# Performance work log

Hardware: AMD Instinct MI355X
Metric: run time of the kernel (lower is better)

The kernel has to match this reference:

```python
import jax, jax.numpy as jnp
import numpy as np

N = 10000        # total_node
IN_SIZE = 128
OUT_SIZE = 128


def setup_inputs() -> dict:
    key = jax.random.key(0)
    k_adj, k_x, k_wn, k_ws = jax.random.split(key, 4)
    adj = jax.random.uniform(k_adj, (N, N), dtype=jnp.float32)           # package[1]
    old_node_embedding = jax.random.normal(k_x, (N, IN_SIZE), dtype=jnp.float32)
    # nn.Linear weights are stored [out, in]
    W_nei = jax.random.normal(k_wn, (OUT_SIZE, IN_SIZE), dtype=jnp.float32) * (1.0 / np.sqrt(IN_SIZE))
    W_self = jax.random.normal(k_ws, (OUT_SIZE, IN_SIZE), dtype=jnp.float32) * (1.0 / np.sqrt(IN_SIZE))
    return {
        "adj": adj,
        "old_node_embedding": old_node_embedding,
        "W_nei": W_nei,
        "W_self": W_self,
        "out_size": OUT_SIZE,
        "use_divce": 0,
    }


def reference(adj, old_node_embedding, W_nei, W_self, out_size, use_divce):
    # Vectorized form of the per-node torch loop:
    #   nei_gather[n]   = adj[n, :] @ X                (torch.mm per node)
    #   nei_info[n]     = nei_gather[n] @ W_nei^T      (nei_update1)
    #   self_info[n]    = X[n] @ W_self^T              (self_node_update1)
    #   new_emb[n]      = act(nei_info[n] + self_info[n])
    # active_method fixed to tanh.
    nei_gather = adj @ old_node_embedding                         # [N, in]
    nei_info = nei_gather @ W_nei.T                               # [N, out]
    self_info = old_node_embedding @ W_self.T                     # [N, out]
    return jnp.tanh(nei_info + self_info)
```

## Files before the change

kernel.cpp:

```cpp
#include <hip/hip_runtime.h>
#include <cmath>


#define N_NODES 10000
#define EMB 128
#define XNT_STRIDE 10240
#define KC 800
#define NKCH 13
#define LDSW 40

typedef __bf16 bf16x8 __attribute__((ext_vector_type(8)));
typedef float  f32x4  __attribute__((ext_vector_type(4)));

__device__ __forceinline__ bf16x8 bzero8() {
    bf16x8 v;
#pragma unroll
    for (int i = 0; i < 8; ++i) v[i] = (__bf16)0.0f;
    return v;
}

__global__ __launch_bounds__(256) void prep_kernel(
    const float* __restrict__ X, const float* __restrict__ Wn,
    __bf16* __restrict__ xnt_hi, __bf16* __restrict__ xnt_lo)
{
    __shared__ float Xl[32 * EMB];
    const int tid = threadIdx.x;
    const int n0 = blockIdx.x * 32;

#pragma unroll
    for (int i = 0; i < 4; ++i) {
        int idx = tid + i * 256;
        int r = idx >> 5;
        int c4 = (idx & 31) << 2;
        int row = n0 + r;
        float4 v = make_float4(0.f, 0.f, 0.f, 0.f);
        if (row < N_NODES) v = *(const float4*)(X + (size_t)row * EMB + c4);
        *(float4*)(Xl + r * EMB + c4) = v;
    }
    __syncthreads();

    const int c = tid & 127;
    const int half = tid >> 7;
    const float* wrow = Wn + c * EMB;

    float acc[16];
#pragma unroll
    for (int r = 0; r < 16; ++r) acc[r] = 0.f;

    for (int k4 = 0; k4 < 32; ++k4) {
        float4 w = *(const float4*)(wrow + k4 * 4);
#pragma unroll
        for (int r = 0; r < 16; ++r) {
            float4 x = *(const float4*)(Xl + (half * 16 + r) * EMB + k4 * 4);
            acc[r] += x.x * w.x + x.y * w.y + x.z * w.z + x.w * w.w;
        }
    }

    if (n0 + half * 16 < N_NODES) {
        bf16x8 h0, h1, l0, l1;
#pragma unroll
        for (int r = 0; r < 16; ++r) {
            float f = acc[r];
            __bf16 h = (__bf16)f;
            __bf16 l = (__bf16)(f - (float)h);
            if (r < 8) { h0[r] = h; l0[r] = l; }
            else       { h1[r - 8] = h; l1[r - 8] = l; }
        }
        size_t base = (size_t)c * XNT_STRIDE + n0 + half * 16;
        *(bf16x8*)(xnt_hi + base)     = h0;
        *(bf16x8*)(xnt_hi + base + 8) = h1;
        *(bf16x8*)(xnt_lo + base)     = l0;
        *(bf16x8*)(xnt_lo + base + 8) = l1;
    }
}

__device__ __forceinline__ void g_load(
    const float* __restrict__ arow_p, bool arv,
    const __bf16* __restrict__ bh_p, const __bf16* __restrict__ bl_p,
    int k0, int kc_end, int akq, int bkq, float4 av[4], bf16x8 bv[4])
{
    int ak = k0 + akq * 16;
#pragma unroll
    for (int i = 0; i < 4; ++i) {
        float4 v = make_float4(0.f, 0.f, 0.f, 0.f);
        int k = ak + i * 4;
        if (arv && k < kc_end) v = *(const float4*)(arow_p + k);
        av[i] = v;
    }
    int bk = k0 + bkq * 16;
    if (bk < kc_end) {
        bv[0] = *(const bf16x8*)(bh_p + bk);
        bv[1] = *(const bf16x8*)(bh_p + bk + 8);
        bv[2] = *(const bf16x8*)(bl_p + bk);
        bv[3] = *(const bf16x8*)(bl_p + bk + 8);
    } else {
        bv[0] = bv[1] = bv[2] = bv[3] = bzero8();
    }
}

__global__ __launch_bounds__(256, 2) void gemm_kernel(
    const float* __restrict__ adj, const __bf16* __restrict__ xnt_hi,
    const __bf16* __restrict__ xnt_lo, float* __restrict__ Ppart)
{
    __shared__ __bf16 Ah[128 * LDSW];
    __shared__ __bf16 Al[128 * LDSW];
    __shared__ __bf16 Bh[128 * LDSW];
    __shared__ __bf16 Bl[128 * LDSW];

    const int tid = threadIdx.x;
    const int m0 = blockIdx.x * 128;
    const int kc0 = blockIdx.y * KC;
    const int kc_end = min(kc0 + KC, N_NODES);
    const int nsub = (kc_end - kc0 + 31) >> 5;

    const int lane = tid & 63;
    const int wave = tid >> 6;
    const int wm = (wave & 1) * 64;
    const int wn = (wave >> 1) * 64;
    const int fr = lane & 15;
    const int q = lane >> 4;

    const int am = tid >> 1, akq = tid & 1;
    const bool arv = (m0 + am) < N_NODES;
    const float* arow_p = adj + (size_t)(m0 + am) * N_NODES;
    const int bc = tid >> 1, bkq = tid & 1;
    const __bf16* bh_p = xnt_hi + (size_t)bc * XNT_STRIDE;
    const __bf16* bl_p = xnt_lo + (size_t)bc * XNT_STRIDE;

    f32x4 acc[4][4];
#pragma unroll
    for (int mt = 0; mt < 4; ++mt)
#pragma unroll
        for (int nt = 0; nt < 4; ++nt)
#pragma unroll
            for (int e = 0; e < 4; ++e) acc[mt][nt][e] = 0.f;

    float4 av[4];
    bf16x8 bv[4];
    g_load(arow_p, arv, bh_p, bl_p, kc0, kc_end, akq, bkq, av, bv);

    for (int ks = 0; ks < nsub; ++ks) {
        bf16x8 ahv[2], alv[2];
#pragma unroll
        for (int i = 0; i < 16; ++i) {
            float f = ((const float*)av)[i];
            __bf16 h = (__bf16)f;
            __bf16 l = (__bf16)(f - (float)h);
            ahv[i >> 3][i & 7] = h;
            alv[i >> 3][i & 7] = l;
        }
        *(bf16x8*)&Ah[am * LDSW + akq * 16]     = ahv[0];
        *(bf16x8*)&Ah[am * LDSW + akq * 16 + 8] = ahv[1];
        *(bf16x8*)&Al[am * LDSW + akq * 16]     = alv[0];
        *(bf16x8*)&Al[am * LDSW + akq * 16 + 8] = alv[1];
        *(bf16x8*)&Bh[bc * LDSW + bkq * 16]     = bv[0];
        *(bf16x8*)&Bh[bc * LDSW + bkq * 16 + 8] = bv[1];
        *(bf16x8*)&Bl[bc * LDSW + bkq * 16]     = bv[2];
        *(bf16x8*)&Bl[bc * LDSW + bkq * 16 + 8] = bv[3];
        __syncthreads();

        float4 av2[4];
        bf16x8 bv2[4];
        g_load(arow_p, arv, bh_p, bl_p, kc0 + (ks + 1) * 32, kc_end, akq, bkq, av2, bv2);

        bf16x8 a_h[4], a_l[4], b_h[4], b_l[4];
#pragma unroll
        for (int t = 0; t < 4; ++t) {
            a_h[t] = *(const bf16x8*)&Ah[(wm + t * 16 + fr) * LDSW + q * 8];
            a_l[t] = *(const bf16x8*)&Al[(wm + t * 16 + fr) * LDSW + q * 8];
            b_h[t] = *(const bf16x8*)&Bh[(wn + t * 16 + fr) * LDSW + q * 8];
            b_l[t] = *(const bf16x8*)&Bl[(wn + t * 16 + fr) * LDSW + q * 8];
        }
#pragma unroll
        for (int mt = 0; mt < 4; ++mt)
#pragma unroll
            for (int nt = 0; nt < 4; ++nt) {
                acc[mt][nt] = __builtin_amdgcn_mfma_f32_16x16x32_bf16(a_h[mt], b_h[nt], acc[mt][nt], 0, 0, 0);
                acc[mt][nt] = __builtin_amdgcn_mfma_f32_16x16x32_bf16(a_h[mt], b_l[nt], acc[mt][nt], 0, 0, 0);
                acc[mt][nt] = __builtin_amdgcn_mfma_f32_16x16x32_bf16(a_l[mt], b_h[nt], acc[mt][nt], 0, 0, 0);
            }
        __syncthreads();
#pragma unroll
        for (int i = 0; i < 4; ++i) { av[i] = av2[i]; bv[i] = bv2[i]; }
    }

    float* P = Ppart + (size_t)blockIdx.y * ((size_t)N_NODES * EMB);
#pragma unroll
    for (int mt = 0; mt < 4; ++mt) {
        int rbase = m0 + wm + mt * 16 + q * 4;
#pragma unroll
        for (int nt = 0; nt < 4; ++nt) {
            int col = wn + nt * 16 + fr;
#pragma unroll
            for (int r = 0; r < 4; ++r) {
                int row = rbase + r;
                if (row < N_NODES)
                    P[(size_t)row * EMB + col] = acc[mt][nt][r];
            }
        }
    }
}

__global__ __launch_bounds__(256) void epi_kernel(
    const float* __restrict__ X, const float* __restrict__ Wself,
    const float* __restrict__ Ppart, float* __restrict__ out)
{
    __shared__ float Xl[32 * EMB];
    const int tid = threadIdx.x;
    const int n0 = blockIdx.x * 32;

#pragma unroll
    for (int i = 0; i < 4; ++i) {
        int idx = tid + i * 256;
        int r = idx >> 5;
        int c4 = (idx & 31) << 2;
        int row = n0 + r;
        float4 v = make_float4(0.f, 0.f, 0.f, 0.f);
        if (row < N_NODES) v = *(const float4*)(X + (size_t)row * EMB + c4);
        *(float4*)(Xl + r * EMB + c4) = v;
    }
    __syncthreads();

    const int c = tid & 127;
    const int half = tid >> 7;
    const float* wrow = Wself + c * EMB;

    float acc[16];
#pragma unroll
    for (int r = 0; r < 16; ++r) acc[r] = 0.f;

    for (int k4 = 0; k4 < 32; ++k4) {
        float4 w = *(const float4*)(wrow + k4 * 4);
#pragma unroll
        for (int r = 0; r < 16; ++r) {
            float4 x = *(const float4*)(Xl + (half * 16 + r) * EMB + k4 * 4);
            acc[r] += x.x * w.x + x.y * w.y + x.z * w.z + x.w * w.w;
        }
    }

    if (n0 + half * 16 < N_NODES) {
        const size_t rb = (size_t)(n0 + half * 16) * EMB + c;
#pragma unroll
        for (int p = 0; p < NKCH; ++p) {
            const float* Pp = Ppart + (size_t)p * ((size_t)N_NODES * EMB) + rb;
#pragma unroll
            for (int r = 0; r < 16; ++r)
                acc[r] += Pp[(size_t)r * EMB];
        }
#pragma unroll
        for (int r = 0; r < 16; ++r)
            out[rb + (size_t)r * EMB] = tanhf(acc[r]);
    }
}

__global__ __launch_bounds__(256) void gemm0_kernel(
    const float* __restrict__ adj, const float* __restrict__ X,
    float* __restrict__ Y)
{
    __shared__ float As[128 * 33];
    __shared__ float Xs[32 * 132];
    const int tid = threadIdx.x;
    const int m0 = blockIdx.x * 128;
    const int kc0 = blockIdx.y * KC;
    const int kc_end = min(kc0 + KC, N_NODES);
    const int nsub = (kc_end - kc0 + 31) >> 5;

    const int am = tid >> 1, akq = tid & 1;
    const bool arv = (m0 + am) < N_NODES;
    const float* arow_p = adj + (size_t)(m0 + am) * N_NODES;
    const int xr = tid >> 3, xq = tid & 7;
    const int mq = tid >> 4, nq = tid & 15;

    float acc[8][8];
#pragma unroll
    for (int i = 0; i < 8; ++i)
#pragma unroll
        for (int j = 0; j < 8; ++j) acc[i][j] = 0.f;

    for (int ks = 0; ks < nsub; ++ks) {
        int k0 = kc0 + ks * 32;
#pragma unroll
        for (int i = 0; i < 4; ++i) {
            int k = k0 + akq * 16 + i * 4;
            float4 v = make_float4(0.f, 0.f, 0.f, 0.f);
            if (arv && k < kc_end) v = *(const float4*)(arow_p + k);
            float* d = As + am * 33 + akq * 16 + i * 4;
            d[0] = v.x; d[1] = v.y; d[2] = v.z; d[3] = v.w;
        }
#pragma unroll
        for (int i = 0; i < 4; ++i) {
            int c0 = xq * 16 + i * 4;
            int krow = k0 + xr;
            float4 v = make_float4(0.f, 0.f, 0.f, 0.f);
            if (krow < kc_end) v = *(const float4*)(X + (size_t)krow * EMB + c0);
            *(float4*)(Xs + xr * 132 + c0) = v;
        }
        __syncthreads();
        for (int k = 0; k < 32; ++k) {
            float a8[8];
#pragma unroll
            for (int i = 0; i < 8; ++i) a8[i] = As[(mq * 8 + i) * 33 + k];
            float4 x0 = *(const float4*)(Xs + k * 132 + nq * 8);
            float4 x1 = *(const float4*)(Xs + k * 132 + nq * 8 + 4);
            float x8[8] = { x0.x, x0.y, x0.z, x0.w, x1.x, x1.y, x1.z, x1.w };
#pragma unroll
            for (int i = 0; i < 8; ++i)
#pragma unroll
                for (int j = 0; j < 8; ++j) acc[i][j] += a8[i] * x8[j];
        }
        __syncthreads();
    }
#pragma unroll
    for (int i = 0; i < 8; ++i) {
        int row = m0 + mq * 8 + i;
        if (row < N_NODES) {
#pragma unroll
            for (int j = 0; j < 8; ++j)
                atomicAdd(Y + (size_t)row * EMB + nq * 8 + j, acc[i][j]);
        }
    }
}

__global__ __launch_bounds__(256) void epi0_kernel(
    const float* __restrict__ X, const float* __restrict__ Wn,
    const float* __restrict__ Ws, float* __restrict__ out)
{
    __shared__ float Xl[32 * EMB];
    __shared__ float Yl[32 * EMB];
    const int tid = threadIdx.x;
    const int n0 = blockIdx.x * 32;

#pragma unroll
    for (int i = 0; i < 4; ++i) {
        int idx = tid + i * 256;
        int r = idx >> 5;
        int c4 = (idx & 31) << 2;
        int row = n0 + r;
        float4 vx = make_float4(0.f, 0.f, 0.f, 0.f);
        float4 vy = vx;
        if (row < N_NODES) {
            vx = *(const float4*)(X + (size_t)row * EMB + c4);
            vy = *(const float4*)(out + (size_t)row * EMB + c4);
        }
        *(float4*)(Xl + r * EMB + c4) = vx;
        *(float4*)(Yl + r * EMB + c4) = vy;
    }
    __syncthreads();

    const int c = tid & 127;
    const int half = tid >> 7;
    const float* wn = Wn + c * EMB;
    const float* ws = Ws + c * EMB;

    float accn[16], accs[16];
#pragma unroll
    for (int r = 0; r < 16; ++r) { accn[r] = 0.f; accs[r] = 0.f; }

    for (int k4 = 0; k4 < 32; ++k4) {
        float4 a = *(const float4*)(wn + k4 * 4);
        float4 b = *(const float4*)(ws + k4 * 4);
#pragma unroll
        for (int r = 0; r < 16; ++r) {
            float4 y = *(const float4*)(Yl + (half * 16 + r) * EMB + k4 * 4);
            float4 x = *(const float4*)(Xl + (half * 16 + r) * EMB + k4 * 4);
            accn[r] += y.x * a.x + y.y * a.y + y.z * a.z + y.w * a.w;
            accs[r] += x.x * b.x + x.y * b.y + x.z * b.z + x.w * b.w;
        }
    }
#pragma unroll
    for (int r = 0; r < 16; ++r) {
        int row = n0 + half * 16 + r;
        if (row < N_NODES)
            out[(size_t)row * EMB + c] = tanhf(accn[r] + accs[r]);
    }
}

extern "C" void kernel_launch(void* const* d_in, const int* in_sizes, int n_in,
                              void* d_out, int out_size, void* d_ws, size_t ws_size,
                              hipStream_t stream) {
    const float* adj = (const float*)d_in[0];
    const float* X   = (const float*)d_in[1];
    const float* Wn  = (const float*)d_in[2];
    const float* Ws  = (const float*)d_in[3];
    float* out = (float*)d_out;

    const size_t xnt_elems = (size_t)EMB * XNT_STRIDE;
    const size_t xnt_bytes = xnt_elems * 2 * sizeof(unsigned short);
    const size_t part_bytes = (size_t)NKCH * N_NODES * EMB * sizeof(float);

    if (ws_size >= xnt_bytes + part_bytes) {
        __bf16* xh = (__bf16*)d_ws;
        __bf16* xl = xh + xnt_elems;
        float* Ppart = (float*)((char*)d_ws + xnt_bytes);
        prep_kernel<<<(N_NODES + 31) / 32, 256, 0, stream>>>(X, Wn, xh, xl);
        gemm_kernel<<<dim3((N_NODES + 127) / 128, NKCH), 256, 0, stream>>>(adj, xh, xl, Ppart);
        epi_kernel<<<(N_NODES + 31) / 32, 256, 0, stream>>>(X, Ws, Ppart, out);
    } else {
        hipMemsetAsync(d_out, 0, (size_t)N_NODES * EMB * sizeof(float), stream);
        gemm0_kernel<<<dim3((N_NODES + 127) / 128, NKCH), 256, 0, stream>>>(adj, X, out);
        epi0_kernel<<<(N_NODES + 31) / 32, 256, 0, stream>>>(X, Wn, Ws, out);
    }
}
```

Baseline: 636.5 us.

## Load MFMA fragments directly from global memory, dropping LDS staging and barriers

The GEMM kernel no longer stages adj and X tiles through shared memory. Each lane now loads its own MFMA fragment rows straight from global memory into registers, splits them into bf16 hi/lo in place, and double-buffers in registers, which removes both __syncthreads per k-step. The split-K chunk grows (fewer partial chunks), which shrinks the partial-sum traffic and the reduction. In exchange, adj data is loaded redundantly by the two waves that share the same rows (and B by the two waves sharing columns), and the accesses are less coalesced, so more global or L2 traffic is expected.

```diff
diff --git a/kernel.cpp b/kernel.cpp
--- a/kernel.cpp
+++ b/kernel.cpp
@@ -5,9 +5,8 @@
 #define N_NODES 10000
 #define EMB 128
 #define XNT_STRIDE 10240
-#define KC 800
-#define NKCH 13
-#define LDSW 40
+#define KC 1440
+#define NKCH 7
 
 typedef __bf16 bf16x8 __attribute__((ext_vector_type(8)));
 typedef float  f32x4  __attribute__((ext_vector_type(4)));
@@ -17,6 +16,17 @@
 #pragma unroll
     for (int i = 0; i < 8; ++i) v[i] = (__bf16)0.0f;
     return v;
+}
+
+__device__ __forceinline__ void split8(const float4& x0, const float4& x1,
+                                       bf16x8& h, bf16x8& l) {
+    float f[8] = {x0.x, x0.y, x0.z, x0.w, x1.x, x1.y, x1.z, x1.w};
+#pragma unroll
+    for (int i = 0; i < 8; ++i) {
+        __bf16 hh = (__bf16)f[i];
+        h[i] = hh;
+        l[i] = (__bf16)(f[i] - (float)hh);
+    }
 }
 
 __global__ __launch_bounds__(256) void prep_kernel(
@@ -74,27 +84,34 @@
     }
 }
 
-__device__ __forceinline__ void g_load(
-    const float* __restrict__ arow_p, bool arv,
-    const __bf16* __restrict__ bh_p, const __bf16* __restrict__ bl_p,
-    int k0, int kc_end, int akq, int bkq, float4 av[4], bf16x8 bv[4])
-{
-    int ak = k0 + akq * 16;
-#pragma unroll
-    for (int i = 0; i < 4; ++i) {
-        float4 v = make_float4(0.f, 0.f, 0.f, 0.f);
-        int k = ak + i * 4;
-        if (arv && k < kc_end) v = *(const float4*)(arow_p + k);
-        av[i] = v;
-    }
-    int bk = k0 + bkq * 16;
-    if (bk < kc_end) {
-        bv[0] = *(const bf16x8*)(bh_p + bk);
-        bv[1] = *(const bf16x8*)(bh_p + bk + 8);
-        bv[2] = *(const bf16x8*)(bl_p + bk);
-        bv[3] = *(const bf16x8*)(bl_p + bk + 8);
-    } else {
-        bv[0] = bv[1] = bv[2] = bv[3] = bzero8();
+struct SubTile {
+    float4 a0[4], a1[4];
+    bf16x8 bh[4], bl[4];
+};
+
+__device__ __forceinline__ void load_sub(
+    const float* const (&arow)[4], const bool (&arv)[4],
+    const __bf16* const (&bhp)[4], const __bf16* const (&blp)[4],
+    int k, int kc_end, SubTile& s)
+{
+    const bool kv = k < kc_end;
+#pragma unroll
+    for (int t = 0; t < 4; ++t) {
+        float4 v0 = make_float4(0.f, 0.f, 0.f, 0.f);
+        float4 v1 = v0;
+        if (kv && arv[t]) {
+            v0 = *(const float4*)(arow[t] + k);
+            v1 = *(const float4*)(arow[t] + k + 4);
+        }
+        s.a0[t] = v0;
+        s.a1[t] = v1;
+        bf16x8 h = bzero8(), l = bzero8();
+        if (kv) {
+            h = *(const bf16x8*)(bhp[t] + k);
+            l = *(const bf16x8*)(blp[t] + k);
+        }
+        s.bh[t] = h;
+        s.bl[t] = l;
     }
 }
 
@@ -102,11 +119,6 @@
     const float* __restrict__ adj, const __bf16* __restrict__ xnt_hi,
     const __bf16* __restrict__ xnt_lo, float* __restrict__ Ppart)
 {
-    __shared__ __bf16 Ah[128 * LDSW];
-    __shared__ __bf16 Al[128 * LDSW];
-    __shared__ __bf16 Bh[128 * LDSW];
-    __shared__ __bf16 Bl[128 * LDSW];
-
     const int tid = threadIdx.x;
     const int m0 = blockIdx.x * 128;
     const int kc0 = blockIdx.y * KC;
@@ -118,14 +130,22 @@
     const int wm = (wave & 1) * 64;
     const int wn = (wave >> 1) * 64;
     const int fr = lane & 15;
-    const int q = lane >> 4;
-
-    const int am = tid >> 1, akq = tid & 1;
-    const bool arv = (m0 + am) < N_NODES;
-    const float* arow_p = adj + (size_t)(m0 + am) * N_NODES;
-    const int bc = tid >> 1, bkq = tid & 1;
-    const __bf16* bh_p = xnt_hi + (size_t)bc * XNT_STRIDE;
-    const __bf16* bl_p = xnt_lo + (size_t)bc * XNT_STRIDE;
+    const int q  = lane >> 4;
+    const int q8 = q * 8;
+
+    const float* arow[4];
+    bool arv[4];
+    const __bf16* bhp[4];
+    const __bf16* blp[4];
+#pragma unroll
+    for (int t = 0; t < 4; ++t) {
+        int row = m0 + wm + t * 16 + fr;
+        arv[t] = row < N_NODES;
+        arow[t] = adj + (size_t)(arv[t] ? row : 0) * N_NODES;
+        int col = wn + t * 16 + fr;
+        bhp[t] = xnt_hi + (size_t)col * XNT_STRIDE;
+        blp[t] = xnt_lo + (size_t)col * XNT_STRIDE;
+    }
 
     f32x4 acc[4][4];
 #pragma unroll
@@ -135,53 +155,25 @@
 #pragma unroll
             for (int e = 0; e < 4; ++e) acc[mt][nt][e] = 0.f;
 
-    float4 av[4];
-    bf16x8 bv[4];
-    g_load(arow_p, arv, bh_p, bl_p, kc0, kc_end, akq, bkq, av, bv);
+    SubTile cur, nxt;
+    load_sub(arow, arv, bhp, blp, kc0 + q8, kc_end, cur);
 
     for (int ks = 0; ks < nsub; ++ks) {
-        bf16x8 ahv[2], alv[2];
-#pragma unroll
-        for (int i = 0; i < 16; ++i) {
-            float f = ((const float*)av)[i];
-            __bf16 h = (__bf16)f;
-            __bf16 l = (__bf16)(f - (float)h);
-            ahv[i >> 3][i & 7] = h;
-            alv[i >> 3][i & 7] = l;
-        }
-        *(bf16x8*)&Ah[am * LDSW + akq * 16]     = ahv[0];
-        *(bf16x8*)&Ah[am * LDSW + akq * 16 + 8] = ahv[1];
-        *(bf16x8*)&Al[am * LDSW + akq * 16]     = alv[0];
-        *(bf16x8*)&Al[am * LDSW + akq * 16 + 8] = alv[1];
-        *(bf16x8*)&Bh[bc * LDSW + bkq * 16]     = bv[0];
-        *(bf16x8*)&Bh[bc * LDSW + bkq * 16 + 8] = bv[1];
-        *(bf16x8*)&Bl[bc * LDSW + bkq * 16]     = bv[2];
-        *(bf16x8*)&Bl[bc * LDSW + bkq * 16 + 8] = bv[3];
-        __syncthreads();
-
-        float4 av2[4];
-        bf16x8 bv2[4];
-        g_load(arow_p, arv, bh_p, bl_p, kc0 + (ks + 1) * 32, kc_end, akq, bkq, av2, bv2);
-
-        bf16x8 a_h[4], a_l[4], b_h[4], b_l[4];
-#pragma unroll
-        for (int t = 0; t < 4; ++t) {
-            a_h[t] = *(const bf16x8*)&Ah[(wm + t * 16 + fr) * LDSW + q * 8];
-            a_l[t] = *(const bf16x8*)&Al[(wm + t * 16 + fr) * LDSW + q * 8];
-            b_h[t] = *(const bf16x8*)&Bh[(wn + t * 16 + fr) * LDSW + q * 8];
-            b_l[t] = *(const bf16x8*)&Bl[(wn + t * 16 + fr) * LDSW + q * 8];
-        }
+        load_sub(arow, arv, bhp, blp, kc0 + (ks + 1) * 32 + q8, kc_end, nxt);
+
+        bf16x8 ah[4], al[4];
+#pragma unroll
+        for (int t = 0; t < 4; ++t) split8(cur.a0[t], cur.a1[t], ah[t], al[t]);
+
 #pragma unroll
         for (int mt = 0; mt < 4; ++mt)
 #pragma unroll
             for (int nt = 0; nt < 4; ++nt) {
-                acc[mt][nt] = __builtin_amdgcn_mfma_f32_16x16x32_bf16(a_h[mt], b_h[nt], acc[mt][nt], 0, 0, 0);
-                acc[mt][nt] = __builtin_amdgcn_mfma_f32_16x16x32_bf16(a_h[mt], b_l[nt], acc[mt][nt], 0, 0, 0);
-                acc[mt][nt] = __builtin_amdgcn_mfma_f32_16x16x32_bf16(a_l[mt], b_h[nt], acc[mt][nt], 0, 0, 0);
+                acc[mt][nt] = __builtin_amdgcn_mfma_f32_16x16x32_bf16(ah[mt], cur.bh[nt], acc[mt][nt], 0, 0, 0);
+                acc[mt][nt] = __builtin_amdgcn_mfma_f32_16x16x32_bf16(ah[mt], cur.bl[nt], acc[mt][nt], 0, 0, 0);
+                acc[mt][nt] = __builtin_amdgcn_mfma_f32_16x16x32_bf16(al[mt], cur.bh[nt], acc[mt][nt], 0, 0, 0);
             }
-        __syncthreads();
-#pragma unroll
-        for (int i = 0; i < 4; ++i) { av[i] = av2[i]; bv[i] = bv2[i]; }
+        cur = nxt;
     }
 
     float* P = Ppart + (size_t)blockIdx.y * ((size_t)N_NODES * EMB);
```

Measured after the change: 765.3 us. 1.2x slower.
